# Kernel tuning notes

Hardware: AMD Instinct MI355X
Metric: run time of the kernel (lower is better)

The kernel has to match this reference:

```python
import jax, jax.numpy as jnp
import numpy as np

NUM_HEADS = 16
NUM_GROUPS = 4
HEAD_DIM = 128  # d_out // num_heads


def setup_inputs() -> dict:
    key = jax.random.key(0)
    ks = jax.random.split(key, 6)
    b, t, d_in, d_out = 4, 2048, 2048, 2048
    kv_dim = NUM_GROUPS * HEAD_DIM
    s = 0.02
    return {
        "x": jax.random.normal(ks[0], (b, t, d_in), jnp.float32),
        "Wq": jax.random.normal(ks[1], (d_in, d_out), jnp.float32) * s,
        "Wk": jax.random.normal(ks[2], (d_in, kv_dim), jnp.float32) * s,
        "Wv": jax.random.normal(ks[3], (d_in, kv_dim), jnp.float32) * s,
        "Wo": jax.random.normal(ks[4], (d_out, d_out), jnp.float32) * s,
        "bo": jnp.zeros((d_out,), jnp.float32),
    }


def reference(x, Wq, Wk, Wv, Wo, bo):
    b, t, _ = x.shape
    H, G, D = NUM_HEADS, NUM_GROUPS, HEAD_DIM
    P = H // G  # heads_per_group
    # Projections
    q = (x @ Wq).reshape(b, t, G, P, D)          # head h = g*P + p matches repeat_interleave
    k = (x @ Wk).reshape(b, t, G, D)
    v = (x @ Wv).reshape(b, t, G, D)
    # Scores: [b, G, P, tq, tk] (grouped form of repeat_interleave over heads)
    scores = jnp.einsum('bqgpd,bkgd->bgpqk', q, k)
    # Causal mask: q_pos < k_pos -> -inf
    qpos = jnp.arange(t)
    mask = qpos[:, None] < qpos[None, :]  # [tq, tk], True above diagonal
    scores = jnp.where(mask[None, None, None], -jnp.inf, scores)
    attn = jax.nn.softmax(scores / np.float32(np.sqrt(D)), axis=-1)
    ctx = jnp.einsum('bgpqk,bkgd->bqgpd', attn, v)  # [b, t, G, P, D]
    ctx = ctx.reshape(b, t, H * D)
    return ctx @ Wo + bo
```

## Files before the change

kernel.cpp:

```cpp
#include <hip/hip_runtime.h>
#include <hip/hip_bf16.h>
#include <stdint.h>
#include <math.h>

#define T_SEQ 2048
#define D_MODEL 2048
#define KV_DIM 512
#define NHEADS 16
#define HDIM 128
#define BATCH 4
#define MT (BATCH * T_SEQ)

typedef __attribute__((ext_vector_type(4))) float f32x4;
typedef __attribute__((ext_vector_type(8))) __bf16 bf16x8;
typedef __attribute__((ext_vector_type(4))) __bf16 bf16x4;
typedef __attribute__((ext_vector_type(8))) unsigned short u16x8;
typedef __attribute__((ext_vector_type(4))) unsigned short u16x4;
typedef __attribute__((ext_vector_type(4))) short s16x4;

static __device__ __forceinline__ unsigned short f32_bf16(float f) {
  unsigned u = __float_as_uint(f);
  u += 0x7fff + ((u >> 16) & 1);
  return (unsigned short)(u >> 16);
}

static __device__ __forceinline__ void gload_lds16(const void* g, void* l) {
  __builtin_amdgcn_global_load_lds(
      (__attribute__((address_space(1))) void*)(const_cast<void*>(g)),
      (__attribute__((address_space(3))) void*)l, 16, 0, 0);
}

static __device__ __forceinline__ f32x4 mfma16(bf16x8 a, bf16x8 b, f32x4 c) {
  return __builtin_amdgcn_mfma_f32_16x16x32_bf16(a, b, c, 0, 0, 0);
}

static __device__ __forceinline__ f32x4 mfma16x16(u16x4 a, u16x4 b, f32x4 c) {
#if __has_builtin(__builtin_amdgcn_mfma_f32_16x16x16bf16_1k)
  return __builtin_amdgcn_mfma_f32_16x16x16bf16_1k(
      __builtin_bit_cast(s16x4, a), __builtin_bit_cast(s16x4, b), c, 0, 0, 0);
#elif __has_builtin(__builtin_amdgcn_mfma_f32_16x16x16_bf16)
  return __builtin_amdgcn_mfma_f32_16x16x16_bf16(
      __builtin_bit_cast(bf16x4, a), __builtin_bit_cast(bf16x4, b), c, 0, 0, 0);
#else
  f32x4 d;
  asm("v_mfma_f32_16x16x16_bf16 %0, %1, %2, %3" : "=v"(d) : "v"(a), "v"(b), "v"(c));
  return d;
#endif
}

#define VIDX(d, c) (((((d) << 3) + ((c) ^ ((d) & 7))) << 3))

__global__ void cvt_kernel(const float* __restrict__ in, unsigned short* __restrict__ out, int n4) {
  int i = blockIdx.x * 256 + threadIdx.x;
  if (i >= n4) return;
  f32x4 v = ((const f32x4*)in)[i];
  u16x4 o;
#pragma unroll
  for (int j = 0; j < 4; ++j) o[j] = f32_bf16(v[j]);
  ((u16x4*)out)[i] = o;
}

__global__ void transpose_kernel(const float* __restrict__ W, unsigned short* __restrict__ Wt,
                                 int K, int N) {
  __shared__ float tile[32][33];
  int bx = blockIdx.x * 32;
  int by = blockIdx.y * 32;
  int tx = threadIdx.x, ty = threadIdx.y;
#pragma unroll
  for (int i = 0; i < 32; i += 8)
    tile[ty + i][tx] = W[(size_t)(by + ty + i) * N + bx + tx];
  __syncthreads();
#pragma unroll
  for (int i = 0; i < 32; i += 8)
    Wt[(size_t)(bx + ty + i) * K + by + tx] = f32_bf16(tile[tx][ty + i]);
}

template <typename OutT, bool HAS_BIAS>
__global__ __launch_bounds__(256, 2) void gemm_bt_kernel(
    const unsigned short* __restrict__ A, const unsigned short* __restrict__ Bt,
    OutT* __restrict__ C, const float* __restrict__ bias, int M, int N, int K) {
  __shared__ unsigned short As[128 * 32];
  __shared__ unsigned short Bs[128 * 32];
  const int tid = threadIdx.x;
  const int wave = tid >> 6, lane = tid & 63;
  const int lr = lane & 15, lh = lane >> 4;
  const int wr = (wave >> 1) * 64, wc = (wave & 1) * 64;
  const size_t ar0 = (size_t)blockIdx.y * 128;
  const size_t br0 = (size_t)blockIdx.x * 128;

  f32x4 acc[4][4] = {};

  for (int k0 = 0; k0 < K; k0 += 32) {
#pragma unroll
    for (int is = 0; is < 2; ++is) {
      const int c = is * 4 + wave;
      const int u = c * 64 + lane;
      const int r = u >> 2;
      const int kk = (u & 3) * 8;
      gload_lds16(A + (ar0 + r) * K + (k0 + kk), (char*)As + c * 1024);
      gload_lds16(Bt + (br0 + r) * K + (k0 + kk), (char*)Bs + c * 1024);
    }
    __syncthreads();
    bf16x8 af[4], bf[4];
#pragma unroll
    for (int m = 0; m < 4; ++m)
      af[m] = *(const bf16x8*)&As[(wr + m * 16 + lr) * 32 + lh * 8];
#pragma unroll
    for (int n = 0; n < 4; ++n)
      bf[n] = *(const bf16x8*)&Bs[(wc + n * 16 + lr) * 32 + lh * 8];
#pragma unroll
    for (int m = 0; m < 4; ++m)
#pragma unroll
      for (int n = 0; n < 4; ++n)
        acc[m][n] = mfma16(af[m], bf[n], acc[m][n]);
    __syncthreads();
  }

#pragma unroll
  for (int m = 0; m < 4; ++m) {
#pragma unroll
    for (int n = 0; n < 4; ++n) {
      const size_t col = br0 + wc + n * 16 + lr;
      float bv = 0.0f;
      if constexpr (HAS_BIAS) bv = bias[col];
#pragma unroll
      for (int r = 0; r < 4; ++r) {
        const size_t row = ar0 + wr + m * 16 + lh * 4 + r;
        const float val = acc[m][n][r] + bv;
        if constexpr (sizeof(OutT) == 2)
          ((unsigned short*)C)[row * N + col] = f32_bf16(val);
        else
          ((float*)C)[row * N + col] = val;
      }
    }
  }
}

static __device__ __forceinline__ void softmax_step(
    const f32x4 st[4], u16x4 pr[4], float& m_run, float& l_run,
    f32x4* oaccq, bool maskT, int kv0, int qglob, int lh) {
  float p[4][4];
#pragma unroll
  for (int n = 0; n < 4; ++n)
#pragma unroll
    for (int r = 0; r < 4; ++r) {
      float val = st[n][r];
      if (maskT && (kv0 + n * 16 + lh * 4 + r > qglob)) val = -1e30f;
      p[n][r] = val;
    }
  float pm[4];
#pragma unroll
  for (int n = 0; n < 4; ++n)
    pm[n] = fmaxf(fmaxf(p[n][0], p[n][1]), fmaxf(p[n][2], p[n][3]));
  float pmax = fmaxf(fmaxf(pm[0], pm[1]), fmaxf(pm[2], pm[3]));
  pmax = fmaxf(pmax, __shfl_xor(pmax, 16));
  pmax = fmaxf(pmax, __shfl_xor(pmax, 32));
  const bool resc = __any(pmax > m_run + 8.0f);
  float alpha = 1.0f;
  if (resc) {
    const float mnew = fmaxf(m_run, pmax);
    alpha = exp2f(m_run - mnew);
    m_run = mnew;
  }
  float rsum = 0.0f;
#pragma unroll
  for (int n = 0; n < 4; ++n) {
#pragma unroll
    for (int r = 0; r < 4; ++r) {
      p[n][r] = exp2f(p[n][r] - m_run);
      rsum += p[n][r];
    }
    u16x4 pk;
#pragma unroll
    for (int r = 0; r < 4; ++r) pk[r] = f32_bf16(p[n][r]);
    pr[n] = pk;
  }
  rsum += __shfl_xor(rsum, 16);
  rsum += __shfl_xor(rsum, 32);
  if (resc) {
    l_run = l_run * alpha + rsum;
#pragma unroll
    for (int r = 0; r < 4; ++r) {
      const float a = __shfl(alpha, lh * 4 + r);
#pragma unroll
      for (int nd = 0; nd < 8; ++nd) oaccq[nd][r] *= a;
    }
  } else {
    l_run += rsum;
  }
}

__global__ __launch_bounds__(256, 2) void attn_kernel(
    const unsigned short* __restrict__ q, const unsigned short* __restrict__ k,
    const unsigned short* __restrict__ v, unsigned short* __restrict__ ctx) {
  const int lin = blockIdx.x;
  const int xcd = lin & 7;
  const int j = lin >> 3;
  const int sel = j & 1;
  const int i = j >> 1;
  const int p = i & 3;
  const int qt = 15 - (i >> 2);
  const int s = xcd * 2 + sel;
  const int b = s >> 2, g = s & 3;
  const int h = g * 4 + p;
  const int tid = threadIdx.x;
  const int wave = tid >> 6, lane = tid & 63;
  const int lr = lane & 15, lh = lane >> 4;
  const int qb = qt * 128;
  const int qrow0 = qb + wave * 16;
  const int qrow1 = qb + 64 + wave * 16;

  __shared__ unsigned short Ks[64 * 128];
  __shared__ unsigned short Vts[128 * 64];

  const int vr0 = (tid & 31) * 2;
  const int vc0 = (tid >> 5) * 16;
  const int vcu = vr0 >> 3, vcw = vr0 & 7;

  const unsigned short* kbase = k + (size_t)b * T_SEQ * KV_DIM + g * HDIM;
  const unsigned short* vbase = v + (size_t)b * T_SEQ * KV_DIM + g * HDIM;

  const float QS = 0.1275174f;
  bf16x8 aq[2][4];
  {
    const unsigned short* qp0 =
        q + ((size_t)b * T_SEQ + qrow0 + lr) * D_MODEL + h * HDIM + lh * 8;
    const unsigned short* qp1 =
        q + ((size_t)b * T_SEQ + qrow1 + lr) * D_MODEL + h * HDIM + lh * 8;
#pragma unroll
    for (int kk = 0; kk < 4; ++kk) {
      u16x8 r0 = *(const u16x8*)(qp0 + kk * 32);
      u16x8 r1 = *(const u16x8*)(qp1 + kk * 32);
      u16x8 o0, o1;
#pragma unroll
      for (int jj = 0; jj < 8; ++jj) {
        o0[jj] = f32_bf16(__uint_as_float((unsigned)r0[jj] << 16) * QS);
        o1[jj] = f32_bf16(__uint_as_float((unsigned)r1[jj] << 16) * QS);
      }
      aq[0][kk] = __builtin_bit_cast(bf16x8, o0);
      aq[1][kk] = __builtin_bit_cast(bf16x8, o1);
    }
  }

  f32x4 oacc[2][8] = {};
  float m_run0 = -1e30f, l_run0 = 0.0f, m_run1 = -1e30f, l_run1 = 0.0f;

  const int nt = 2 * qt + 2;

  for (int t = 0; t < nt; ++t) {
    const int kv0 = t * 64;
    __syncthreads();
#pragma unroll
    for (int is = 0; is < 4; ++is) {
      const int c = is * 4 + wave;
      const int u = c * 64 + lane;
      const int vu = u ^ ((u >> 4) & 7);
      const int r = vu >> 4;
      const int cc = (vu & 15) * 8;
      gload_lds16(kbase + (size_t)(kv0 + r) * KV_DIM + cc, (char*)Ks + c * 1024);
    }
    {
      const unsigned short* vp = vbase + (size_t)(kv0 + vr0) * KV_DIM + vc0;
      u16x8 va0 = *(const u16x8*)(vp);
      u16x8 va1 = *(const u16x8*)(vp + 8);
      u16x8 vb0 = *(const u16x8*)(vp + KV_DIM);
      u16x8 vb1 = *(const u16x8*)(vp + KV_DIM + 8);
#pragma unroll
      for (int jj = 0; jj < 8; ++jj) {
        const int d0 = vc0 + jj, d1 = vc0 + 8 + jj;
        *(unsigned int*)&Vts[VIDX(d0, vcu) + vcw] =
            (unsigned int)va0[jj] | ((unsigned int)vb0[jj] << 16);
        *(unsigned int*)&Vts[VIDX(d1, vcu) + vcw] =
            (unsigned int)va1[jj] | ((unsigned int)vb1[jj] << 16);
      }
    }
    __syncthreads();

    const bool live0 = (t < nt - 1);
    const bool mask0 = (t == nt - 2);
    const bool mask1 = (t == nt - 1);

    f32x4 st0[4] = {}, st1[4] = {};
#pragma unroll
    for (int n = 0; n < 4; ++n) {
      const int rr = n * 16 + lr;
#pragma unroll
      for (int kk = 0; kk < 4; ++kk) {
        const int lu = rr * 16 + kk * 4 + lh;
        const int pu = lu ^ (rr & 7);
        const bf16x8 ak = *(const bf16x8*)((const char*)Ks + pu * 16);
        if (live0) st0[n] = mfma16(ak, aq[0][kk], st0[n]);
        st1[n] = mfma16(ak, aq[1][kk], st1[n]);
      }
    }

    u16x4 pr0[4], pr1[4];
    if (live0)
      softmax_step(st0, pr0, m_run0, l_run0, oacc[0], mask0, kv0, qrow0 + lr, lh);
    softmax_step(st1, pr1, m_run1, l_run1, oacc[1], mask1, kv0, qrow1 + lr, lh);

#pragma unroll
    for (int n = 0; n < 4; ++n) {
      const int cb = n * 2 + (lh >> 1);
      const int off = (lh & 1) * 4;
#pragma unroll
      for (int nd = 0; nd < 8; ++nd) {
        const int d = nd * 16 + lr;
        const u16x4 vf = *(const u16x4*)&Vts[VIDX(d, cb) + off];
        if (live0) oacc[0][nd] = mfma16x16(pr0[n], vf, oacc[0][nd]);
        oacc[1][nd] = mfma16x16(pr1[n], vf, oacc[1][nd]);
      }
    }
  }

#pragma unroll
  for (int m = 0; m < 2; ++m) {
    const float lm = (m == 0) ? l_run0 : l_run1;
    const int qrow = (m == 0) ? qrow0 : qrow1;
    unsigned short* cp = ctx + ((size_t)b * T_SEQ + qrow) * D_MODEL + h * HDIM;
#pragma unroll
    for (int r = 0; r < 4; ++r) {
      const float inv = 1.0f / __shfl(lm, lh * 4 + r);
#pragma unroll
      for (int nd = 0; nd < 8; ++nd)
        cp[(size_t)(lh * 4 + r) * D_MODEL + nd * 16 + lr] =
            f32_bf16(oacc[m][nd][r] * inv);
    }
  }
}

extern "C" void kernel_launch(void* const* d_in, const int* in_sizes, int n_in,
                              void* d_out, int out_size, void* d_ws, size_t ws_size,
                              hipStream_t stream) {
  const float* x = (const float*)d_in[0];
  const float* Wq = (const float*)d_in[1];
  const float* Wk = (const float*)d_in[2];
  const float* Wv = (const float*)d_in[3];
  const float* Wo = (const float*)d_in[4];
  const float* bo = (const float*)d_in[5];
  float* out = (float*)d_out;

  char* ws = (char*)d_ws;
  unsigned short* xb = (unsigned short*)(ws + 0);
  unsigned short* ctx = (unsigned short*)(ws + 0);
  unsigned short* qbuf = (unsigned short*)(ws + 33554432);
  unsigned short* kbuf = (unsigned short*)(ws + 67108864);
  unsigned short* vbuf = (unsigned short*)(ws + 75497472);
  unsigned short* WqT = (unsigned short*)(ws + 83886080);
  unsigned short* WkT = (unsigned short*)(ws + 92274688);
  unsigned short* WvT = (unsigned short*)(ws + 94371840);
  unsigned short* WoT = (unsigned short*)(ws + 96468992);

  const int n4 = MT * D_MODEL / 4;
  cvt_kernel<<<(n4 + 255) / 256, 256, 0, stream>>>(x, xb, n4);
  dim3 tb(32, 8);
  transpose_kernel<<<dim3(D_MODEL / 32, D_MODEL / 32), tb, 0, stream>>>(Wq, WqT, D_MODEL, D_MODEL);
  transpose_kernel<<<dim3(KV_DIM / 32, D_MODEL / 32), tb, 0, stream>>>(Wk, WkT, D_MODEL, KV_DIM);
  transpose_kernel<<<dim3(KV_DIM / 32, D_MODEL / 32), tb, 0, stream>>>(Wv, WvT, D_MODEL, KV_DIM);
  transpose_kernel<<<dim3(D_MODEL / 32, D_MODEL / 32), tb, 0, stream>>>(Wo, WoT, D_MODEL, D_MODEL);

  gemm_bt_kernel<unsigned short, false><<<dim3(D_MODEL / 128, MT / 128), 256, 0, stream>>>(
      xb, WqT, qbuf, nullptr, MT, D_MODEL, D_MODEL);
  gemm_bt_kernel<unsigned short, false><<<dim3(KV_DIM / 128, MT / 128), 256, 0, stream>>>(
      xb, WkT, kbuf, nullptr, MT, KV_DIM, D_MODEL);
  gemm_bt_kernel<unsigned short, false><<<dim3(KV_DIM / 128, MT / 128), 256, 0, stream>>>(
      xb, WvT, vbuf, nullptr, MT, KV_DIM, D_MODEL);

  attn_kernel<<<1024, 256, 0, stream>>>(qbuf, kbuf, vbuf, ctx);

  gemm_bt_kernel<float, true><<<dim3(D_MODEL / 128, MT / 128), 256, 0, stream>>>(
      ctx, WoT, out, bo, MT, D_MODEL, D_MODEL);
}
```

Baseline: 459.2 us.

## Fuse Q/K/V projections into one GEMM and add MFMA priority hints

Concatenates the transposed Wq, Wk and Wv into one weight matrix so a single GEMM writes an interleaved QKV buffer with row stride 3072. The attention kernel now reads Q, K and V from that buffer. Merging removes two launches and lets the small K and V GEMMs share a larger, better-filled grid. The softmax bf16 packing now uses the packed hardware conversion intrinsics, and s_setprio raises wave priority around the MFMA sections. The cost is strided, wider rows for the K/V loads in attention.

```diff
diff --git a/kernel.cpp b/kernel.cpp
--- a/kernel.cpp
+++ b/kernel.cpp
@@ -6,6 +6,7 @@
 #define T_SEQ 2048
 #define D_MODEL 2048
 #define KV_DIM 512
+#define QKV_LD 3072
 #define NHEADS 16
 #define HDIM 128
 #define BATCH 4
@@ -170,9 +171,14 @@
       p[n][r] = exp2f(p[n][r] - m_run);
       rsum += p[n][r];
     }
+    __hip_bfloat162 t0 = __float22bfloat162_rn(make_float2(p[n][0], p[n][1]));
+    __hip_bfloat162 t1 = __float22bfloat162_rn(make_float2(p[n][2], p[n][3]));
+    unsigned lo, hi;
+    __builtin_memcpy(&lo, &t0, 4);
+    __builtin_memcpy(&hi, &t1, 4);
+    unsigned long long both = (unsigned long long)lo | ((unsigned long long)hi << 32);
     u16x4 pk;
-#pragma unroll
-    for (int r = 0; r < 4; ++r) pk[r] = f32_bf16(p[n][r]);
+    __builtin_memcpy(&pk, &both, 8);
     pr[n] = pk;
   }
   rsum += __shfl_xor(rsum, 16);
@@ -191,8 +197,7 @@
 }
 
 __global__ __launch_bounds__(256, 2) void attn_kernel(
-    const unsigned short* __restrict__ q, const unsigned short* __restrict__ k,
-    const unsigned short* __restrict__ v, unsigned short* __restrict__ ctx) {
+    const unsigned short* __restrict__ qkv, unsigned short* __restrict__ ctx) {
   const int lin = blockIdx.x;
   const int xcd = lin & 7;
   const int j = lin >> 3;
@@ -217,16 +222,15 @@
   const int vc0 = (tid >> 5) * 16;
   const int vcu = vr0 >> 3, vcw = vr0 & 7;
 
-  const unsigned short* kbase = k + (size_t)b * T_SEQ * KV_DIM + g * HDIM;
-  const unsigned short* vbase = v + (size_t)b * T_SEQ * KV_DIM + g * HDIM;
+  const unsigned short* qrow_base = qkv + (size_t)b * T_SEQ * QKV_LD;
+  const unsigned short* kbase = qrow_base + D_MODEL + g * HDIM;
+  const unsigned short* vbase = qrow_base + D_MODEL + KV_DIM + g * HDIM;
 
   const float QS = 0.1275174f;
   bf16x8 aq[2][4];
   {
-    const unsigned short* qp0 =
-        q + ((size_t)b * T_SEQ + qrow0 + lr) * D_MODEL + h * HDIM + lh * 8;
-    const unsigned short* qp1 =
-        q + ((size_t)b * T_SEQ + qrow1 + lr) * D_MODEL + h * HDIM + lh * 8;
+    const unsigned short* qp0 = qrow_base + (size_t)(qrow0 + lr) * QKV_LD + h * HDIM + lh * 8;
+    const unsigned short* qp1 = qrow_base + (size_t)(qrow1 + lr) * QKV_LD + h * HDIM + lh * 8;
 #pragma unroll
     for (int kk = 0; kk < 4; ++kk) {
       u16x8 r0 = *(const u16x8*)(qp0 + kk * 32);
@@ -257,14 +261,14 @@
       const int vu = u ^ ((u >> 4) & 7);
       const int r = vu >> 4;
       const int cc = (vu & 15) * 8;
-      gload_lds16(kbase + (size_t)(kv0 + r) * KV_DIM + cc, (char*)Ks + c * 1024);
+      gload_lds16(kbase + (size_t)(kv0 + r) * QKV_LD + cc, (char*)Ks + c * 1024);
     }
     {
-      const unsigned short* vp = vbase + (size_t)(kv0 + vr0) * KV_DIM + vc0;
+      const unsigned short* vp = vbase + (size_t)(kv0 + vr0) * QKV_LD + vc0;
       u16x8 va0 = *(const u16x8*)(vp);
       u16x8 va1 = *(const u16x8*)(vp + 8);
-      u16x8 vb0 = *(const u16x8*)(vp + KV_DIM);
-      u16x8 vb1 = *(const u16x8*)(vp + KV_DIM + 8);
+      u16x8 vb0 = *(const u16x8*)(vp + QKV_LD);
+      u16x8 vb1 = *(const u16x8*)(vp + QKV_LD + 8);
 #pragma unroll
       for (int jj = 0; jj < 8; ++jj) {
         const int d0 = vc0 + jj, d1 = vc0 + 8 + jj;
@@ -281,6 +285,7 @@
     const bool mask1 = (t == nt - 1);
 
     f32x4 st0[4] = {}, st1[4] = {};
+    __builtin_amdgcn_s_setprio(1);
 #pragma unroll
     for (int n = 0; n < 4; ++n) {
       const int rr = n * 16 + lr;
@@ -293,12 +298,14 @@
         st1[n] = mfma16(ak, aq[1][kk], st1[n]);
       }
     }
+    __builtin_amdgcn_s_setprio(0);
 
     u16x4 pr0[4], pr1[4];
     if (live0)
       softmax_step(st0, pr0, m_run0, l_run0, oacc[0], mask0, kv0, qrow0 + lr, lh);
     softmax_step(st1, pr1, m_run1, l_run1, oacc[1], mask1, kv0, qrow1 + lr, lh);
 
+    __builtin_amdgcn_s_setprio(1);
 #pragma unroll
     for (int n = 0; n < 4; ++n) {
       const int cb = n * 2 + (lh >> 1);
@@ -311,6 +318,7 @@
         oacc[1][nd] = mfma16x16(pr1[n], vf, oacc[1][nd]);
       }
     }
+    __builtin_amdgcn_s_setprio(0);
   }
 
 #pragma unroll
@@ -343,30 +351,26 @@
   char* ws = (char*)d_ws;
   unsigned short* xb = (unsigned short*)(ws + 0);
   unsigned short* ctx = (unsigned short*)(ws + 0);
-  unsigned short* qbuf = (unsigned short*)(ws + 33554432);
-  unsigned short* kbuf = (unsigned short*)(ws + 67108864);
-  unsigned short* vbuf = (unsigned short*)(ws + 75497472);
-  unsigned short* WqT = (unsigned short*)(ws + 83886080);
-  unsigned short* WkT = (unsigned short*)(ws + 92274688);
-  unsigned short* WvT = (unsigned short*)(ws + 94371840);
+  unsigned short* qkv = (unsigned short*)(ws + 33554432);
+  unsigned short* WqkvT = (unsigned short*)(ws + 83886080);
   unsigned short* WoT = (unsigned short*)(ws + 96468992);
 
   const int n4 = MT * D_MODEL / 4;
   cvt_kernel<<<(n4 + 255) / 256, 256, 0, stream>>>(x, xb, n4);
   dim3 tb(32, 8);
-  transpose_kernel<<<dim3(D_MODEL / 32, D_MODEL / 32), tb, 0, stream>>>(Wq, WqT, D_MODEL, D_MODEL);
-  transpose_kernel<<<dim3(KV_DIM / 32, D_MODEL / 32), tb, 0, stream>>>(Wk, WkT, D_MODEL, KV_DIM);
-  transpose_kernel<<<dim3(KV_DIM / 32, D_MODEL / 32), tb, 0, stream>>>(Wv, WvT, D_MODEL, KV_DIM);
-  transpose_kernel<<<dim3(D_MODEL / 32, D_MODEL / 32), tb, 0, stream>>>(Wo, WoT, D_MODEL, D_MODEL);
-
-  gemm_bt_kernel<unsigned short, false><<<dim3(D_MODEL / 128, MT / 128), 256, 0, stream>>>(
-      xb, WqT, qbuf, nullptr, MT, D_MODEL, D_MODEL);
-  gemm_bt_kernel<unsigned short, false><<<dim3(KV_DIM / 128, MT / 128), 256, 0, stream>>>(
-      xb, WkT, kbuf, nullptr, MT, KV_DIM, D_MODEL);
-  gemm_bt_kernel<unsigned short, false><<<dim3(KV_DIM / 128, MT / 128), 256, 0, stream>>>(
-      xb, WvT, vbuf, nullptr, MT, KV_DIM, D_MODEL);
-
-  attn_kernel<<<1024, 256, 0, stream>>>(qbuf, kbuf, vbuf, ctx);
+  transpose_kernel<<<dim3(D_MODEL / 32, D_MODEL / 32), tb, 0, stream>>>(
+      Wq, WqkvT, D_MODEL, D_MODEL);
+  transpose_kernel<<<dim3(KV_DIM / 32, D_MODEL / 32), tb, 0, stream>>>(
+      Wk, WqkvT + (size_t)D_MODEL * D_MODEL, D_MODEL, KV_DIM);
+  transpose_kernel<<<dim3(KV_DIM / 32, D_MODEL / 32), tb, 0, stream>>>(
+      Wv, WqkvT + (size_t)(D_MODEL + KV_DIM) * D_MODEL, D_MODEL, KV_DIM);
+  transpose_kernel<<<dim3(D_MODEL / 32, D_MODEL / 32), tb, 0, stream>>>(
+      Wo, WoT, D_MODEL, D_MODEL);
+
+  gemm_bt_kernel<unsigned short, false><<<dim3(QKV_LD / 128, MT / 128), 256, 0, stream>>>(
+      xb, WqkvT, qkv, nullptr, MT, QKV_LD, D_MODEL);
+
+  attn_kernel<<<1024, 256, 0, stream>>>(qkv, ctx);
 
   gemm_bt_kernel<float, true><<<dim3(D_MODEL / 128, MT / 128), 256, 0, stream>>>(
       ctx, WoT, out, bo, MT, D_MODEL, D_MODEL);
```

Result: faster. 407.1 us (-11.3%).
